# Performance work log

Measured on AMD Instinct MI355X. Metric: run time of the kernel, lower is better.

The kernel has to match this reference:

```python
import jax, jax.numpy as jnp
import numpy as np
from jax import lax

T, H, I, E, K = 1024, 1024, 512, 16, 4


def setup_inputs() -> dict:
    key = jax.random.key(0)
    k1, k2, k3, k4, k5 = jax.random.split(key, 5)
    hidden_states = jax.random.normal(k1, (T, H), dtype=jnp.float32)
    top_k_index = jax.random.randint(k2, (T, K), 0, E)
    top_k_weights = jax.random.uniform(k3, (T, K), dtype=jnp.float32)
    gate_up_proj = jax.random.normal(k4, (E, 2 * I, H), dtype=jnp.float32) * 0.02
    down_proj = jax.random.normal(k5, (E, H, I), dtype=jnp.float32) * 0.02
    return {
        "hidden_states": hidden_states,
        "top_k_index": top_k_index,
        "top_k_weights": top_k_weights,
        "gate_up_proj": gate_up_proj,
        "down_proj": down_proj,
    }


def reference(hidden_states, top_k_index, top_k_weights, gate_up_proj, down_proj):
    num_experts = gate_up_proj.shape[0]
    # combine[t, e] = sum_k top_k_weights[t, k] * [top_k_index[t, k] == e]
    # Expert output is linear in the routing weight, so summing weights over
    # duplicate (token, expert) hits matches the original index_add_ exactly.
    one_hot = jax.nn.one_hot(top_k_index, num_experts, dtype=hidden_states.dtype)  # [T, K, E]
    combine = jnp.einsum("tke,tk->te", one_hot, top_k_weights)  # [T, E]

    def expert_step(acc, xs):
        w_gu, w_d, c = xs  # [2I, H], [H, I], [T]
        gu = hidden_states @ w_gu.T          # [T, 2I]
        gate, up = jnp.split(gu, 2, axis=-1)
        h = jax.nn.silu(gate) * up            # [T, I]
        out = h @ w_d.T                       # [T, H]
        return acc + out * c[:, None], None

    final, _ = lax.scan(
        expert_step,
        jnp.zeros_like(hidden_states),
        (gate_up_proj, down_proj, combine.T),
    )
    return final
```

## Files before the change

### kernel.cpp

```cpp
#include <hip/hip_runtime.h>
#include <hip/hip_bf16.h>
#include <cstdint>
#include <cstddef>

#define T_TOK 1024
#define HDIM  1024
#define IDIM  512
#define NEXP  16
#define TOPK  4
#define CAP   1024

typedef __bf16 bf16;
typedef __attribute__((ext_vector_type(8))) __bf16 bf16x8;
typedef __attribute__((ext_vector_type(4))) __bf16 bf16x4;
typedef __attribute__((ext_vector_type(4))) float f32x4;

#define BAR() __builtin_amdgcn_s_barrier()
#define SB()  __builtin_amdgcn_sched_barrier(0)
#define LGKM0() asm volatile("s_waitcnt lgkmcnt(0)" ::: "memory")
#define WAIT_VM4 asm volatile("s_waitcnt vmcnt(4)" ::: "memory")
#define WAIT_VM0 asm volatile("s_waitcnt vmcnt(0)" ::: "memory")

__device__ __forceinline__ void lds_load16(void* lds_dst, const void* g_src) {
  __builtin_amdgcn_global_load_lds(
      (__attribute__((address_space(1))) unsigned int*)(void*)(g_src),
      (__attribute__((address_space(3))) unsigned int*)(lds_dst),
      16, 0, 0);
}

__device__ __forceinline__ bf16x4 cvt4(float4 a) {
  bf16x4 o;
  o[0] = (bf16)a.x; o[1] = (bf16)a.y; o[2] = (bf16)a.z; o[3] = (bf16)a.w;
  return o;
}


#define CVT_BLOCKS (T_TOK * HDIM / 4 / 256)

__global__ void prep_kernel(const float* __restrict__ hid_f, bf16* __restrict__ hid_b,
                            const int* __restrict__ idx, const float* __restrict__ w,
                            int* __restrict__ etk, float* __restrict__ ew,
                            int* __restrict__ cntpad) {
  __shared__ int cnt;
  const int b = blockIdx.x;
  const int tid = threadIdx.x;
  if (b < CVT_BLOCKS) {
    int i = b * 256 + tid;
    float4 v = ((const float4*)hid_f)[i];
    ((bf16x4*)hid_b)[i] = cvt4(v);
    if (b == 0)
      ((bf16x4*)(hid_b + (size_t)T_TOK * HDIM))[tid] = cvt4(make_float4(0.f, 0.f, 0.f, 0.f));
    return;
  }
  const int e = b - CVT_BLOCKS;
  if (tid == 0) cnt = 0;
  __syncthreads();
  for (int j = tid; j < T_TOK * TOPK; j += blockDim.x) {
    if (idx[j] == e) {
      int slot = atomicAdd(&cnt, 1);
      if (slot < CAP) { etk[e * CAP + slot] = j; ew[e * CAP + slot] = w[j]; }
    }
  }
  __syncthreads();
  int c = cnt < CAP ? cnt : CAP;
  int p = (c + 127) & ~127;
  for (int j = c + tid; j < p; j += blockDim.x) {
    etk[e * CAP + j] = (T_TOK << 2);
    ew[e * CAP + j] = 0.f;
  }
  if (tid == 0) cntpad[e] = p;
}


__global__ __launch_bounds__(256, 3) void gemm1_kernel(
    const bf16* __restrict__ hid,
    const float* __restrict__ gup,
    const int* __restrict__ etk, const float* __restrict__ ew,
    const int* __restrict__ cntpad,
    bf16* __restrict__ hsc) {
  __shared__ __align__(16) bf16 As[2][128 * 64];
  __shared__ __align__(16) bf16 Bs[2][64 * 64];
  const int e = blockIdx.y, z = blockIdx.z;
  const int ntiles = cntpad[e] >> 7;
  const int n0 = blockIdx.x * 32;
  const int ebase = e * CAP;
  const int tid = threadIdx.x, lane = tid & 63, wid = tid >> 6;
  const int wm = (wid >> 1) * 64, wi = (wid & 1) * 16;
  const int lcol = lane & 15, lquad = lane >> 4;
  const int l7 = lcol & 7;
  const int srow = tid >> 3;
  const int swz = ((tid & 7) ^ (srow & 7)) * 8;
  const int r = tid >> 2;
  const int c0 = (tid & 3) * 4;
  const int grow = (r < 32) ? (n0 + r) : (IDIM + n0 + (r - 32));
  const float* gB = gup + (size_t)e * (2 * IDIM) * HDIM + (size_t)grow * HDIM + c0;
  int wb[4];
#pragma unroll
  for (int j = 0; j < 4; ++j) {
    int c = c0 + 16 * j;
    wb[j] = (((c >> 3) ^ (r & 7)) * 8) + (c & 7);
  }
  const int bst = r * 64;

  for (int mt = z; mt < ntiles; mt += 3) {
    const int mrow = ebase + mt * 128;
    const bf16* gA[4];
#pragma unroll
    for (int q = 0; q < 4; ++q)
      gA[q] = hid + (size_t)(etk[mrow + srow + 32 * q] >> 2) * HDIM + swz;
    f32x4 aG[4], aU[4];
#pragma unroll
    for (int mf = 0; mf < 4; ++mf) {
      aG[mf] = f32x4{0.f, 0.f, 0.f, 0.f};
      aU[mf] = f32x4{0.f, 0.f, 0.f, 0.f};
    }
    float4 bvA[4], bvB[4];

#pragma unroll
    for (int j = 0; j < 4; ++j) bvA[j] = *(const float4*)(gB + 16 * j);
    SB();
#pragma unroll
    for (int q = 0; q < 4; ++q)
      lds_load16(&As[0][tid * 8 + q * 2048], gA[q]);
    SB();
#pragma unroll
    for (int j = 0; j < 4; ++j) bvB[j] = *(const float4*)(gB + 64 + 16 * j);
    SB();

    auto STEP = [&](int k, int cur, float4 (&bcur)[4]) {
      const int nxt = cur ^ 1;
      if (k == 15) { WAIT_VM0; } else { WAIT_VM4; }
      SB();
#pragma unroll
      for (int j = 0; j < 4; ++j)
        *(bf16x4*)&Bs[cur][bst + wb[j]] = cvt4(bcur[j]);
      LGKM0();
      SB();
      BAR();
      SB();
      if (k + 1 < 16) {
#pragma unroll
        for (int q = 0; q < 4; ++q)
          lds_load16(&As[nxt][tid * 8 + q * 2048], gA[q] + (k + 1) * 64);
      }
      SB();
      if (k + 2 < 16) {
#pragma unroll
        for (int j = 0; j < 4; ++j)
          bcur[j] = *(const float4*)(gB + (k + 2) * 64 + 16 * j);
      }
      SB();
#pragma unroll
      for (int ks = 0; ks < 2; ++ks) {
        const int sw = ((ks * 4 + lquad) ^ l7) * 8;
        bf16x8 bg = *(const bf16x8*)&Bs[cur][(wi + lcol) * 64 + sw];
        bf16x8 bu = *(const bf16x8*)&Bs[cur][(32 + wi + lcol) * 64 + sw];
#pragma unroll
        for (int mf = 0; mf < 4; ++mf) {
          bf16x8 af = *(const bf16x8*)&As[cur][(wm + mf * 16 + lcol) * 64 + sw];
          aG[mf] = __builtin_amdgcn_mfma_f32_16x16x32_bf16(af, bg, aG[mf], 0, 0, 0);
          aU[mf] = __builtin_amdgcn_mfma_f32_16x16x32_bf16(af, bu, aU[mf], 0, 0, 0);
        }
      }
    };
#pragma unroll
    for (int kk = 0; kk < 8; ++kk) {
      STEP(2 * kk,     0, bvA);
      STEP(2 * kk + 1, 1, bvB);
    }
#pragma unroll
    for (int mf = 0; mf < 4; ++mf) {
#pragma unroll
      for (int rr = 0; rr < 4; ++rr) {
        const int erow = mt * 128 + wm + mf * 16 + lquad * 4 + rr;
        const float wgt = ew[ebase + erow];
        float g = aG[mf][rr], u = aU[mf][rr];
        float s = g / (1.f + __expf(-g));
        hsc[(size_t)(ebase + erow) * IDIM + n0 + wi + lcol] = (bf16)(s * u * wgt);
      }
    }
  }
}


__global__ __launch_bounds__(256, 3) void gemm2_kernel(
    const bf16* __restrict__ hsc,
    const float* __restrict__ down,
    const int* __restrict__ etk, const int* __restrict__ cntpad,
    bf16* __restrict__ slabs) {
  __shared__ __align__(16) bf16 As[2][128 * 64];
  __shared__ __align__(16) bf16 Bs[2][64 * 64];
  const int e = blockIdx.y, z = blockIdx.z;
  const int ntiles = cntpad[e] >> 7;
  const int n0 = blockIdx.x * 64;
  const int ebase = e * CAP;
  const int tid = threadIdx.x, lane = tid & 63, wid = tid >> 6;
  const int wm = (wid >> 1) * 64, wh = (wid & 1) * 32;
  const int lcol = lane & 15, lquad = lane >> 4;
  const int l7 = lcol & 7;
  const int srow = tid >> 3;
  const int swz = ((tid & 7) ^ (srow & 7)) * 8;
  const int r = tid >> 2;
  const int c0 = (tid & 3) * 4;
  const float* gB = down + (size_t)e * HDIM * IDIM + (size_t)(n0 + r) * IDIM + c0;
  int wb[4];
#pragma unroll
  for (int j = 0; j < 4; ++j) {
    int c = c0 + 16 * j;
    wb[j] = (((c >> 3) ^ (r & 7)) * 8) + (c & 7);
  }
  const int bst = r * 64;

  for (int mt = z; mt < ntiles; mt += 3) {
    const size_t rbase = (size_t)(ebase + mt * 128);
    const bf16* gA[4];
#pragma unroll
    for (int q = 0; q < 4; ++q)
      gA[q] = hsc + (rbase + srow + 32 * q) * IDIM + swz;
    f32x4 acc[4][2];
#pragma unroll
    for (int mf = 0; mf < 4; ++mf) {
      acc[mf][0] = f32x4{0.f, 0.f, 0.f, 0.f};
      acc[mf][1] = f32x4{0.f, 0.f, 0.f, 0.f};
    }
    float4 bvA[4], bvB[4];
#pragma unroll
    for (int j = 0; j < 4; ++j) bvA[j] = *(const float4*)(gB + 16 * j);
    SB();
#pragma unroll
    for (int q = 0; q < 4; ++q)
      lds_load16(&As[0][tid * 8 + q * 2048], gA[q]);
    SB();
#pragma unroll
    for (int j = 0; j < 4; ++j) bvB[j] = *(const float4*)(gB + 64 + 16 * j);
    SB();

    auto STEP = [&](int k, int cur, float4 (&bcur)[4]) {
      const int nxt = cur ^ 1;
      if (k == 7) { WAIT_VM0; } else { WAIT_VM4; }
      SB();
#pragma unroll
      for (int j = 0; j < 4; ++j)
        *(bf16x4*)&Bs[cur][bst + wb[j]] = cvt4(bcur[j]);
      LGKM0();
      SB();
      BAR();
      SB();
      if (k + 1 < 8) {
#pragma unroll
        for (int q = 0; q < 4; ++q)
          lds_load16(&As[nxt][tid * 8 + q * 2048], gA[q] + (k + 1) * 64);
      }
      SB();
      if (k + 2 < 8) {
#pragma unroll
        for (int j = 0; j < 4; ++j)
          bcur[j] = *(const float4*)(gB + (k + 2) * 64 + 16 * j);
      }
      SB();
#pragma unroll
      for (int ks = 0; ks < 2; ++ks) {
        const int sw = ((ks * 4 + lquad) ^ l7) * 8;
        bf16x8 b0 = *(const bf16x8*)&Bs[cur][(wh + lcol) * 64 + sw];
        bf16x8 b1 = *(const bf16x8*)&Bs[cur][(wh + 16 + lcol) * 64 + sw];
#pragma unroll
        for (int mf = 0; mf < 4; ++mf) {
          bf16x8 af = *(const bf16x8*)&As[cur][(wm + mf * 16 + lcol) * 64 + sw];
          acc[mf][0] = __builtin_amdgcn_mfma_f32_16x16x32_bf16(af, b0, acc[mf][0], 0, 0, 0);
          acc[mf][1] = __builtin_amdgcn_mfma_f32_16x16x32_bf16(af, b1, acc[mf][1], 0, 0, 0);
        }
      }
    };
#pragma unroll
    for (int kk = 0; kk < 4; ++kk) {
      STEP(2 * kk,     0, bvA);
      STEP(2 * kk + 1, 1, bvB);
    }
#pragma unroll
    for (int mf = 0; mf < 4; ++mf) {
#pragma unroll
      for (int rr = 0; rr < 4; ++rr) {
        const int tk = etk[ebase + mt * 128 + wm + mf * 16 + lquad * 4 + rr];
        const int tok = tk >> 2, kslot = tk & 3;
        bf16* orow = slabs + ((size_t)kslot * (T_TOK + 1) + tok) * HDIM + n0 + wh + lcol;
        orow[0]  = (bf16)acc[mf][0][rr];
        orow[16] = (bf16)acc[mf][1][rr];
      }
    }
  }
}


__global__ void reduce_kernel(const bf16* __restrict__ slabs, float* __restrict__ out) {
  const size_t stride8 = (size_t)(T_TOK + 1) * HDIM / 8;
  int i = blockIdx.x * blockDim.x + threadIdx.x;
  bf16x8 a = ((const bf16x8*)slabs)[i];
  bf16x8 b = ((const bf16x8*)slabs)[i + stride8];
  bf16x8 c = ((const bf16x8*)slabs)[i + 2 * stride8];
  bf16x8 d = ((const bf16x8*)slabs)[i + 3 * stride8];
  float4 o0, o1;
  float r[8];
#pragma unroll
  for (int j = 0; j < 8; ++j)
    r[j] = (float)a[j] + (float)b[j] + (float)c[j] + (float)d[j];
  o0.x = r[0]; o0.y = r[1]; o0.z = r[2]; o0.w = r[3];
  o1.x = r[4]; o1.y = r[5]; o1.z = r[6]; o1.w = r[7];
  ((float4*)out)[i * 2]     = o0;
  ((float4*)out)[i * 2 + 1] = o1;
}


extern "C" void kernel_launch(void* const* d_in, const int* in_sizes, int n_in,
                              void* d_out, int out_size, void* d_ws, size_t ws_size,
                              hipStream_t stream) {
  const float* hid_f  = (const float*)d_in[0];
  const int*   idx    = (const int*)d_in[1];
  const float* tw     = (const float*)d_in[2];
  const float* gup_f  = (const float*)d_in[3];
  const float* down_f = (const float*)d_in[4];
  float* out = (float*)d_out;

  uint8_t* ws = (uint8_t*)d_ws;
  size_t off = 0;
  bf16* hid_b = (bf16*)(ws + off);   off += (size_t)(T_TOK + 1) * HDIM * 2;
  int*  etk   = (int*)(ws + off);    off += (size_t)NEXP * CAP * 4;
  float* ewt  = (float*)(ws + off);  off += (size_t)NEXP * CAP * 4;
  int* cntpad = (int*)(ws + off);    off += 256;
  bf16* hsc   = (bf16*)(ws + off);   off += (size_t)NEXP * CAP * IDIM * 2;
  bf16* slabs = (bf16*)(ws + off);

  prep_kernel<<<dim3(CVT_BLOCKS + NEXP), dim3(256), 0, stream>>>(
      hid_f, hid_b, idx, tw, etk, ewt, cntpad);
  gemm1_kernel<<<dim3(IDIM / 32, NEXP, 3), dim3(256), 0, stream>>>(
      hid_b, gup_f, etk, ewt, cntpad, hsc);
  gemm2_kernel<<<dim3(HDIM / 64, NEXP, 3), dim3(256), 0, stream>>>(
      hsc, down_f, etk, cntpad, slabs);
  reduce_kernel<<<dim3(T_TOK * HDIM / 8 / 256), dim3(256), 0, stream>>>(slabs, out);
}
```

Measured before the change: 168.4 us.

## Fuse all four MoE stages into one cooperative persistent kernel with grid syncs

Replaces the four separate launches (prep, gate/up GEMM, down GEMM, reduce) with one cooperative kernel of 768 blocks that runs each stage in turn, separated by grid-wide syncs. The GEMM bodies become shared templates. The aim is to cut per-launch overhead and the gaps between kernels. In exchange, each grid.sync has a cost, the cooperative launch needs every block co-resident at 3 blocks per CU, and the prep and reduce stages now run on a fixed grid. The old multi-kernel path stays as a fallback if the cooperative launch fails.

```diff
diff --git a/kernel.cpp b/kernel.cpp
--- a/kernel.cpp
+++ b/kernel.cpp
@@ -1,7 +1,10 @@
 #include <hip/hip_runtime.h>
 #include <hip/hip_bf16.h>
+#include <hip/hip_cooperative_groups.h>
 #include <cstdint>
 #include <cstddef>
+
+namespace cg = cooperative_groups;
 
 #define T_TOK 1024
 #define HDIM  1024
@@ -9,6 +12,7 @@
 #define NEXP  16
 #define TOPK  4
 #define CAP   1024
+#define GRID  768
 
 typedef __bf16 bf16;
 typedef __attribute__((ext_vector_type(8))) __bf16 bf16x8;
@@ -32,6 +36,293 @@
   bf16x4 o;
   o[0] = (bf16)a.x; o[1] = (bf16)a.y; o[2] = (bf16)a.z; o[3] = (bf16)a.w;
   return o;
+}
+
+template <typename LdsA, typename LdsB>
+__device__ __forceinline__ void gemm1_body(
+    LdsA& As, LdsB& Bs, int n0, int e, int z,
+    const bf16* __restrict__ hid, const float* __restrict__ gup,
+    const int* __restrict__ etk, const float* __restrict__ ew,
+    const int* __restrict__ cntpad, bf16* __restrict__ hsc) {
+  const int ntiles = cntpad[e] >> 7;
+  const int ebase = e * CAP;
+  const int tid = threadIdx.x, lane = tid & 63, wid = tid >> 6;
+  const int wm = (wid >> 1) * 64, wi = (wid & 1) * 16;
+  const int lcol = lane & 15, lquad = lane >> 4;
+  const int l7 = lcol & 7;
+  const int srow = tid >> 3;
+  const int swz = ((tid & 7) ^ (srow & 7)) * 8;
+  const int r = tid >> 2;
+  const int c0 = (tid & 3) * 4;
+  const int grow = (r < 32) ? (n0 + r) : (IDIM + n0 + (r - 32));
+  const float* gB = gup + (size_t)e * (2 * IDIM) * HDIM + (size_t)grow * HDIM + c0;
+  int wb[4];
+#pragma unroll
+  for (int j = 0; j < 4; ++j) {
+    int c = c0 + 16 * j;
+    wb[j] = (((c >> 3) ^ (r & 7)) * 8) + (c & 7);
+  }
+  const int bst = r * 64;
+
+  for (int mt = z; mt < ntiles; mt += 3) {
+    const int mrow = ebase + mt * 128;
+    const bf16* gA[4];
+#pragma unroll
+    for (int q = 0; q < 4; ++q)
+      gA[q] = hid + (size_t)(etk[mrow + srow + 32 * q] >> 2) * HDIM + swz;
+    f32x4 aG[4], aU[4];
+#pragma unroll
+    for (int mf = 0; mf < 4; ++mf) {
+      aG[mf] = f32x4{0.f, 0.f, 0.f, 0.f};
+      aU[mf] = f32x4{0.f, 0.f, 0.f, 0.f};
+    }
+    float4 bvA[4], bvB[4];
+#pragma unroll
+    for (int j = 0; j < 4; ++j) bvA[j] = *(const float4*)(gB + 16 * j);
+    SB();
+#pragma unroll
+    for (int q = 0; q < 4; ++q)
+      lds_load16(&As[0][tid * 8 + q * 2048], gA[q]);
+    SB();
+#pragma unroll
+    for (int j = 0; j < 4; ++j) bvB[j] = *(const float4*)(gB + 64 + 16 * j);
+    SB();
+
+    auto STEP = [&](int k, int cur, float4 (&bcur)[4]) {
+      const int nxt = cur ^ 1;
+      if (k == 15) { WAIT_VM0; } else { WAIT_VM4; }
+      SB();
+#pragma unroll
+      for (int j = 0; j < 4; ++j)
+        *(bf16x4*)&Bs[cur][bst + wb[j]] = cvt4(bcur[j]);
+      LGKM0();
+      SB();
+      BAR();
+      SB();
+      if (k + 1 < 16) {
+#pragma unroll
+        for (int q = 0; q < 4; ++q)
+          lds_load16(&As[nxt][tid * 8 + q * 2048], gA[q] + (k + 1) * 64);
+      }
+      SB();
+      if (k + 2 < 16) {
+#pragma unroll
+        for (int j = 0; j < 4; ++j)
+          bcur[j] = *(const float4*)(gB + (k + 2) * 64 + 16 * j);
+      }
+      SB();
+#pragma unroll
+      for (int ks = 0; ks < 2; ++ks) {
+        const int sw = ((ks * 4 + lquad) ^ l7) * 8;
+        bf16x8 bg = *(const bf16x8*)&Bs[cur][(wi + lcol) * 64 + sw];
+        bf16x8 bu = *(const bf16x8*)&Bs[cur][(32 + wi + lcol) * 64 + sw];
+#pragma unroll
+        for (int mf = 0; mf < 4; ++mf) {
+          bf16x8 af = *(const bf16x8*)&As[cur][(wm + mf * 16 + lcol) * 64 + sw];
+          aG[mf] = __builtin_amdgcn_mfma_f32_16x16x32_bf16(af, bg, aG[mf], 0, 0, 0);
+          aU[mf] = __builtin_amdgcn_mfma_f32_16x16x32_bf16(af, bu, aU[mf], 0, 0, 0);
+        }
+      }
+    };
+#pragma unroll
+    for (int kk = 0; kk < 8; ++kk) {
+      STEP(2 * kk,     0, bvA);
+      STEP(2 * kk + 1, 1, bvB);
+    }
+#pragma unroll
+    for (int mf = 0; mf < 4; ++mf) {
+#pragma unroll
+      for (int rr = 0; rr < 4; ++rr) {
+        const int erow = mt * 128 + wm + mf * 16 + lquad * 4 + rr;
+        const float wgt = ew[ebase + erow];
+        float g = aG[mf][rr], u = aU[mf][rr];
+        float s = g / (1.f + __expf(-g));
+        hsc[(size_t)(ebase + erow) * IDIM + n0 + wi + lcol] = (bf16)(s * u * wgt);
+      }
+    }
+  }
+}
+
+template <typename LdsA, typename LdsB>
+__device__ __forceinline__ void gemm2_body(
+    LdsA& As, LdsB& Bs, int n0, int e, int z,
+    const bf16* __restrict__ hsc, const float* __restrict__ down,
+    const int* __restrict__ etk, const int* __restrict__ cntpad,
+    bf16* __restrict__ slabs) {
+  const int ntiles = cntpad[e] >> 7;
+  const int ebase = e * CAP;
+  const int tid = threadIdx.x, lane = tid & 63, wid = tid >> 6;
+  const int wm = (wid >> 1) * 64, wh = (wid & 1) * 32;
+  const int lcol = lane & 15, lquad = lane >> 4;
+  const int l7 = lcol & 7;
+  const int srow = tid >> 3;
+  const int swz = ((tid & 7) ^ (srow & 7)) * 8;
+  const int r = tid >> 2;
+  const int c0 = (tid & 3) * 4;
+  const float* gB = down + (size_t)e * HDIM * IDIM + (size_t)(n0 + r) * IDIM + c0;
+  int wb[4];
+#pragma unroll
+  for (int j = 0; j < 4; ++j) {
+    int c = c0 + 16 * j;
+    wb[j] = (((c >> 3) ^ (r & 7)) * 8) + (c & 7);
+  }
+  const int bst = r * 64;
+
+  for (int mt = z; mt < ntiles; mt += 3) {
+    const size_t rbase = (size_t)(ebase + mt * 128);
+    const bf16* gA[4];
+#pragma unroll
+    for (int q = 0; q < 4; ++q)
+      gA[q] = hsc + (rbase + srow + 32 * q) * IDIM + swz;
+    f32x4 acc[4][2];
+#pragma unroll
+    for (int mf = 0; mf < 4; ++mf) {
+      acc[mf][0] = f32x4{0.f, 0.f, 0.f, 0.f};
+      acc[mf][1] = f32x4{0.f, 0.f, 0.f, 0.f};
+    }
+    float4 bvA[4], bvB[4];
+#pragma unroll
+    for (int j = 0; j < 4; ++j) bvA[j] = *(const float4*)(gB + 16 * j);
+    SB();
+#pragma unroll
+    for (int q = 0; q < 4; ++q)
+      lds_load16(&As[0][tid * 8 + q * 2048], gA[q]);
+    SB();
+#pragma unroll
+    for (int j = 0; j < 4; ++j) bvB[j] = *(const float4*)(gB + 64 + 16 * j);
+    SB();
+
+    auto STEP = [&](int k, int cur, float4 (&bcur)[4]) {
+      const int nxt = cur ^ 1;
+      if (k == 7) { WAIT_VM0; } else { WAIT_VM4; }
+      SB();
+#pragma unroll
+      for (int j = 0; j < 4; ++j)
+        *(bf16x4*)&Bs[cur][bst + wb[j]] = cvt4(bcur[j]);
+      LGKM0();
+      SB();
+      BAR();
+      SB();
+      if (k + 1 < 8) {
+#pragma unroll
+        for (int q = 0; q < 4; ++q)
+          lds_load16(&As[nxt][tid * 8 + q * 2048], gA[q] + (k + 1) * 64);
+      }
+      SB();
+      if (k + 2 < 8) {
+#pragma unroll
+        for (int j = 0; j < 4; ++j)
+          bcur[j] = *(const float4*)(gB + (k + 2) * 64 + 16 * j);
+      }
+      SB();
+#pragma unroll
+      for (int ks = 0; ks < 2; ++ks) {
+        const int sw = ((ks * 4 + lquad) ^ l7) * 8;
+        bf16x8 b0 = *(const bf16x8*)&Bs[cur][(wh + lcol) * 64 + sw];
+        bf16x8 b1 = *(const bf16x8*)&Bs[cur][(wh + 16 + lcol) * 64 + sw];
+#pragma unroll
+        for (int mf = 0; mf < 4; ++mf) {
+          bf16x8 af = *(const bf16x8*)&As[cur][(wm + mf * 16 + lcol) * 64 + sw];
+          acc[mf][0] = __builtin_amdgcn_mfma_f32_16x16x32_bf16(af, b0, acc[mf][0], 0, 0, 0);
+          acc[mf][1] = __builtin_amdgcn_mfma_f32_16x16x32_bf16(af, b1, acc[mf][1], 0, 0, 0);
+        }
+      }
+    };
+#pragma unroll
+    for (int kk = 0; kk < 4; ++kk) {
+      STEP(2 * kk,     0, bvA);
+      STEP(2 * kk + 1, 1, bvB);
+    }
+#pragma unroll
+    for (int mf = 0; mf < 4; ++mf) {
+#pragma unroll
+      for (int rr = 0; rr < 4; ++rr) {
+        const int tk = etk[ebase + mt * 128 + wm + mf * 16 + lquad * 4 + rr];
+        const int tok = tk >> 2, kslot = tk & 3;
+        bf16* orow = slabs + ((size_t)kslot * (T_TOK + 1) + tok) * HDIM + n0 + wh + lcol;
+        orow[0]  = (bf16)acc[mf][0][rr];
+        orow[16] = (bf16)acc[mf][1][rr];
+      }
+    }
+  }
+}
+
+
+__global__ __launch_bounds__(256, 3) void mega_kernel(
+    const float* __restrict__ hid_f, const int* __restrict__ idx,
+    const float* __restrict__ tw, const float* __restrict__ gup,
+    const float* __restrict__ down,
+    bf16* __restrict__ hid_b, int* __restrict__ etk, float* __restrict__ ewt,
+    int* __restrict__ cntpad, bf16* __restrict__ hsc, bf16* __restrict__ slabs,
+    float* __restrict__ out) {
+  __shared__ __align__(16) bf16 As[2][128 * 64];
+  __shared__ __align__(16) bf16 Bs[2][64 * 64];
+  cg::grid_group grid = cg::this_grid();
+  const int bid = blockIdx.x;
+  const int tid = threadIdx.x;
+
+  for (int i = bid * 256 + tid; i < T_TOK * HDIM / 4; i += GRID * 256) {
+    float4 v = ((const float4*)hid_f)[i];
+    ((bf16x4*)hid_b)[i] = cvt4(v);
+  }
+  if (bid == 16)
+    ((bf16x4*)(hid_b + (size_t)T_TOK * HDIM))[tid] = cvt4(make_float4(0.f, 0.f, 0.f, 0.f));
+  if (bid < NEXP) {
+    int* cntp = (int*)&As[0][0];
+    if (tid == 0) *cntp = 0;
+    __syncthreads();
+    for (int j = tid; j < T_TOK * TOPK; j += 256) {
+      if (idx[j] == bid) {
+        int slot = atomicAdd(cntp, 1);
+        if (slot < CAP) { etk[bid * CAP + slot] = j; ewt[bid * CAP + slot] = tw[j]; }
+      }
+    }
+    __syncthreads();
+    int c = *cntp < CAP ? *cntp : CAP;
+    int p = (c + 127) & ~127;
+    for (int j = c + tid; j < p; j += 256) {
+      etk[bid * CAP + j] = (T_TOK << 2);
+      ewt[bid * CAP + j] = 0.f;
+    }
+    if (tid == 0) cntpad[bid] = p;
+  }
+  grid.sync();
+
+  {
+    const int n0 = (bid & 15) * 32;
+    const int e  = (bid >> 4) & 15;
+    const int z  = bid >> 8;
+    gemm1_body(As, Bs, n0, e, z, hid_b, gup, etk, ewt, cntpad, hsc);
+  }
+  grid.sync();
+
+  {
+    const int n0 = (bid & 15) * 64;
+    const int e  = (bid >> 4) & 15;
+    const int z  = bid >> 8;
+    gemm2_body(As, Bs, n0, e, z, hsc, down, etk, cntpad, slabs);
+  }
+  grid.sync();
+
+  {
+    const size_t stride8 = (size_t)(T_TOK + 1) * HDIM / 8;
+    int i = bid * 256 + tid;
+    if (i < T_TOK * HDIM / 8) {
+      bf16x8 a = ((const bf16x8*)slabs)[i];
+      bf16x8 b = ((const bf16x8*)slabs)[i + stride8];
+      bf16x8 c = ((const bf16x8*)slabs)[i + 2 * stride8];
+      bf16x8 d = ((const bf16x8*)slabs)[i + 3 * stride8];
+      float4 o0, o1;
+      float rr[8];
+#pragma unroll
+      for (int j = 0; j < 8; ++j)
+        rr[j] = (float)a[j] + (float)b[j] + (float)c[j] + (float)d[j];
+      o0.x = rr[0]; o0.y = rr[1]; o0.z = rr[2]; o0.w = rr[3];
+      o1.x = rr[4]; o1.y = rr[5]; o1.z = rr[6]; o1.w = rr[7];
+      ((float4*)out)[i * 2]     = o0;
+      ((float4*)out)[i * 2 + 1] = o1;
+    }
+  }
 }
 
 
@@ -71,225 +362,23 @@
   if (tid == 0) cntpad[e] = p;
 }
 
-
 __global__ __launch_bounds__(256, 3) void gemm1_kernel(
-    const bf16* __restrict__ hid,
-    const float* __restrict__ gup,
+    const bf16* __restrict__ hid, const float* __restrict__ gup,
     const int* __restrict__ etk, const float* __restrict__ ew,
-    const int* __restrict__ cntpad,
-    bf16* __restrict__ hsc) {
+    const int* __restrict__ cntpad, bf16* __restrict__ hsc) {
   __shared__ __align__(16) bf16 As[2][128 * 64];
   __shared__ __align__(16) bf16 Bs[2][64 * 64];
-  const int e = blockIdx.y, z = blockIdx.z;
-  const int ntiles = cntpad[e] >> 7;
-  const int n0 = blockIdx.x * 32;
-  const int ebase = e * CAP;
-  const int tid = threadIdx.x, lane = tid & 63, wid = tid >> 6;
-  const int wm = (wid >> 1) * 64, wi = (wid & 1) * 16;
-  const int lcol = lane & 15, lquad = lane >> 4;
-  const int l7 = lcol & 7;
-  const int srow = tid >> 3;
-  const int swz = ((tid & 7) ^ (srow & 7)) * 8;
-  const int r = tid >> 2;
-  const int c0 = (tid & 3) * 4;
-  const int grow = (r < 32) ? (n0 + r) : (IDIM + n0 + (r - 32));
-  const float* gB = gup + (size_t)e * (2 * IDIM) * HDIM + (size_t)grow * HDIM + c0;
-  int wb[4];
-#pragma unroll
-  for (int j = 0; j < 4; ++j) {
-    int c = c0 + 16 * j;
-    wb[j] = (((c >> 3) ^ (r & 7)) * 8) + (c & 7);
-  }
-  const int bst = r * 64;
-
-  for (int mt = z; mt < ntiles; mt += 3) {
-    const int mrow = ebase + mt * 128;
-    const bf16* gA[4];
-#pragma unroll
-    for (int q = 0; q < 4; ++q)
-      gA[q] = hid + (size_t)(etk[mrow + srow + 32 * q] >> 2) * HDIM + swz;
-    f32x4 aG[4], aU[4];
-#pragma unroll
-    for (int mf = 0; mf < 4; ++mf) {
-      aG[mf] = f32x4{0.f, 0.f, 0.f, 0.f};
-      aU[mf] = f32x4{0.f, 0.f, 0.f, 0.f};
-    }
-    float4 bvA[4], bvB[4];
-
-#pragma unroll
-    for (int j = 0; j < 4; ++j) bvA[j] = *(const float4*)(gB + 16 * j);
-    SB();
-#pragma unroll
-    for (int q = 0; q < 4; ++q)
-      lds_load16(&As[0][tid * 8 + q * 2048], gA[q]);
-    SB();
-#pragma unroll
-    for (int j = 0; j < 4; ++j) bvB[j] = *(const float4*)(gB + 64 + 16 * j);
-    SB();
-
-    auto STEP = [&](int k, int cur, float4 (&bcur)[4]) {
-      const int nxt = cur ^ 1;
-      if (k == 15) { WAIT_VM0; } else { WAIT_VM4; }
-      SB();
-#pragma unroll
-      for (int j = 0; j < 4; ++j)
-        *(bf16x4*)&Bs[cur][bst + wb[j]] = cvt4(bcur[j]);
-      LGKM0();
-      SB();
-      BAR();
-      SB();
-      if (k + 1 < 16) {
-#pragma unroll
-        for (int q = 0; q < 4; ++q)
-          lds_load16(&As[nxt][tid * 8 + q * 2048], gA[q] + (k + 1) * 64);
-      }
-      SB();
-      if (k + 2 < 16) {
-#pragma unroll
-        for (int j = 0; j < 4; ++j)
-          bcur[j] = *(const float4*)(gB + (k + 2) * 64 + 16 * j);
-      }
-      SB();
-#pragma unroll
-      for (int ks = 0; ks < 2; ++ks) {
-        const int sw = ((ks * 4 + lquad) ^ l7) * 8;
-        bf16x8 bg = *(const bf16x8*)&Bs[cur][(wi + lcol) * 64 + sw];
-        bf16x8 bu = *(const bf16x8*)&Bs[cur][(32 + wi + lcol) * 64 + sw];
-#pragma unroll
-        for (int mf = 0; mf < 4; ++mf) {
-          bf16x8 af = *(const bf16x8*)&As[cur][(wm + mf * 16 + lcol) * 64 + sw];
-          aG[mf] = __builtin_amdgcn_mfma_f32_16x16x32_bf16(af, bg, aG[mf], 0, 0, 0);
-          aU[mf] = __builtin_amdgcn_mfma_f32_16x16x32_bf16(af, bu, aU[mf], 0, 0, 0);
-        }
-      }
-    };
-#pragma unroll
-    for (int kk = 0; kk < 8; ++kk) {
-      STEP(2 * kk,     0, bvA);
-      STEP(2 * kk + 1, 1, bvB);
-    }
-#pragma unroll
-    for (int mf = 0; mf < 4; ++mf) {
-#pragma unroll
-      for (int rr = 0; rr < 4; ++rr) {
-        const int erow = mt * 128 + wm + mf * 16 + lquad * 4 + rr;
-        const float wgt = ew[ebase + erow];
-        float g = aG[mf][rr], u = aU[mf][rr];
-        float s = g / (1.f + __expf(-g));
-        hsc[(size_t)(ebase + erow) * IDIM + n0 + wi + lcol] = (bf16)(s * u * wgt);
-      }
-    }
-  }
-}
-
+  gemm1_body(As, Bs, blockIdx.x * 32, blockIdx.y, blockIdx.z, hid, gup, etk, ew, cntpad, hsc);
+}
 
 __global__ __launch_bounds__(256, 3) void gemm2_kernel(
-    const bf16* __restrict__ hsc,
-    const float* __restrict__ down,
+    const bf16* __restrict__ hsc, const float* __restrict__ down,
     const int* __restrict__ etk, const int* __restrict__ cntpad,
     bf16* __restrict__ slabs) {
   __shared__ __align__(16) bf16 As[2][128 * 64];
   __shared__ __align__(16) bf16 Bs[2][64 * 64];
-  const int e = blockIdx.y, z = blockIdx.z;
-  const int ntiles = cntpad[e] >> 7;
-  const int n0 = blockIdx.x * 64;
-  const int ebase = e * CAP;
-  const int tid = threadIdx.x, lane = tid & 63, wid = tid >> 6;
-  const int wm = (wid >> 1) * 64, wh = (wid & 1) * 32;
-  const int lcol = lane & 15, lquad = lane >> 4;
-  const int l7 = lcol & 7;
-  const int srow = tid >> 3;
-  const int swz = ((tid & 7) ^ (srow & 7)) * 8;
-  const int r = tid >> 2;
-  const int c0 = (tid & 3) * 4;
-  const float* gB = down + (size_t)e * HDIM * IDIM + (size_t)(n0 + r) * IDIM + c0;
-  int wb[4];
-#pragma unroll
-  for (int j = 0; j < 4; ++j) {
-    int c = c0 + 16 * j;
-    wb[j] = (((c >> 3) ^ (r & 7)) * 8) + (c & 7);
-  }
-  const int bst = r * 64;
-
-  for (int mt = z; mt < ntiles; mt += 3) {
-    const size_t rbase = (size_t)(ebase + mt * 128);
-    const bf16* gA[4];
-#pragma unroll
-    for (int q = 0; q < 4; ++q)
-      gA[q] = hsc + (rbase + srow + 32 * q) * IDIM + swz;
-    f32x4 acc[4][2];
-#pragma unroll
-    for (int mf = 0; mf < 4; ++mf) {
-      acc[mf][0] = f32x4{0.f, 0.f, 0.f, 0.f};
-      acc[mf][1] = f32x4{0.f, 0.f, 0.f, 0.f};
-    }
-    float4 bvA[4], bvB[4];
-#pragma unroll
-    for (int j = 0; j < 4; ++j) bvA[j] = *(const float4*)(gB + 16 * j);
-    SB();
-#pragma unroll
-    for (int q = 0; q < 4; ++q)
-      lds_load16(&As[0][tid * 8 + q * 2048], gA[q]);
-    SB();
-#pragma unroll
-    for (int j = 0; j < 4; ++j) bvB[j] = *(const float4*)(gB + 64 + 16 * j);
-    SB();
-
-    auto STEP = [&](int k, int cur, float4 (&bcur)[4]) {
-      const int nxt = cur ^ 1;
-      if (k == 7) { WAIT_VM0; } else { WAIT_VM4; }
-      SB();
-#pragma unroll
-      for (int j = 0; j < 4; ++j)
-        *(bf16x4*)&Bs[cur][bst + wb[j]] = cvt4(bcur[j]);
-      LGKM0();
-      SB();
-      BAR();
-      SB();
-      if (k + 1 < 8) {
-#pragma unroll
-        for (int q = 0; q < 4; ++q)
-          lds_load16(&As[nxt][tid * 8 + q * 2048], gA[q] + (k + 1) * 64);
-      }
-      SB();
-      if (k + 2 < 8) {
-#pragma unroll
-        for (int j = 0; j < 4; ++j)
-          bcur[j] = *(const float4*)(gB + (k + 2) * 64 + 16 * j);
-      }
-      SB();
-#pragma unroll
-      for (int ks = 0; ks < 2; ++ks) {
-        const int sw = ((ks * 4 + lquad) ^ l7) * 8;
-        bf16x8 b0 = *(const bf16x8*)&Bs[cur][(wh + lcol) * 64 + sw];
-        bf16x8 b1 = *(const bf16x8*)&Bs[cur][(wh + 16 + lcol) * 64 + sw];
-#pragma unroll
-        for (int mf = 0; mf < 4; ++mf) {
-          bf16x8 af = *(const bf16x8*)&As[cur][(wm + mf * 16 + lcol) * 64 + sw];
-          acc[mf][0] = __builtin_amdgcn_mfma_f32_16x16x32_bf16(af, b0, acc[mf][0], 0, 0, 0);
-          acc[mf][1] = __builtin_amdgcn_mfma_f32_16x16x32_bf16(af, b1, acc[mf][1], 0, 0, 0);
-        }
-      }
-    };
-#pragma unroll
-    for (int kk = 0; kk < 4; ++kk) {
-      STEP(2 * kk,     0, bvA);
-      STEP(2 * kk + 1, 1, bvB);
-    }
-#pragma unroll
-    for (int mf = 0; mf < 4; ++mf) {
-#pragma unroll
-      for (int rr = 0; rr < 4; ++rr) {
-        const int tk = etk[ebase + mt * 128 + wm + mf * 16 + lquad * 4 + rr];
-        const int tok = tk >> 2, kslot = tk & 3;
-        bf16* orow = slabs + ((size_t)kslot * (T_TOK + 1) + tok) * HDIM + n0 + wh + lcol;
-        orow[0]  = (bf16)acc[mf][0][rr];
-        orow[16] = (bf16)acc[mf][1][rr];
-      }
-    }
-  }
-}
-
+  gemm2_body(As, Bs, blockIdx.x * 64, blockIdx.y, blockIdx.z, hsc, down, etk, cntpad, slabs);
+}
 
 __global__ void reduce_kernel(const bf16* __restrict__ slabs, float* __restrict__ out) {
   const size_t stride8 = (size_t)(T_TOK + 1) * HDIM / 8;
@@ -329,11 +418,20 @@
   bf16* hsc   = (bf16*)(ws + off);   off += (size_t)NEXP * CAP * IDIM * 2;
   bf16* slabs = (bf16*)(ws + off);
 
-  prep_kernel<<<dim3(CVT_BLOCKS + NEXP), dim3(256), 0, stream>>>(
-      hid_f, hid_b, idx, tw, etk, ewt, cntpad);
-  gemm1_kernel<<<dim3(IDIM / 32, NEXP, 3), dim3(256), 0, stream>>>(
-      hid_b, gup_f, etk, ewt, cntpad, hsc);
-  gemm2_kernel<<<dim3(HDIM / 64, NEXP, 3), dim3(256), 0, stream>>>(
-      hsc, down_f, etk, cntpad, slabs);
-  reduce_kernel<<<dim3(T_TOK * HDIM / 8 / 256), dim3(256), 0, stream>>>(slabs, out);
-}
+  void* args[] = {
+    (void*)&hid_f, (void*)&idx, (void*)&tw, (void*)&gup_f, (void*)&down_f,
+    (void*)&hid_b, (void*)&etk, (void*)&ewt, (void*)&cntpad, (void*)&hsc,
+    (void*)&slabs, (void*)&out
+  };
+  hipError_t err = hipLaunchCooperativeKernel(
+      reinterpret_cast<void*>(mega_kernel), dim3(GRID), dim3(256), args, 0, stream);
+  if (err != hipSuccess) {
+    prep_kernel<<<dim3(CVT_BLOCKS + NEXP), dim3(256), 0, stream>>>(
+        hid_f, hid_b, idx, tw, etk, ewt, cntpad);
+    gemm1_kernel<<<dim3(IDIM / 32, NEXP, 3), dim3(256), 0, stream>>>(
+        hid_b, gup_f, etk, ewt, cntpad, hsc);
+    gemm2_kernel<<<dim3(HDIM / 64, NEXP, 3), dim3(256), 0, stream>>>(
+        hsc, down_f, etk, cntpad, slabs);
+    reduce_kernel<<<dim3(T_TOK * HDIM / 8 / 256), dim3(256), 0, stream>>>(slabs, out);
+  }
+}
```

New measurement: 464.4 us. 176% more time.
